# Kernel optimization log

Hardware: AMD Instinct MI355X
Metric: run time of the kernel (lower is better)

Reference implementation:

```python
import jax, jax.numpy as jnp
import numpy as np

B, C, L, MID, HID, OUT, K = 4096, 6, 1024, 512, 512, 256, 5
EPS = 1e-5


def _bn_eval(x, g, b, m, v):
    # BatchNorm1d eval mode on (B, C, T): normalize per channel with running stats
    inv = g / jnp.sqrt(v + EPS)
    return (x - m[None, :, None]) * inv[None, :, None] + b[None, :, None]


def setup_inputs() -> dict:
    key = jax.random.key(0)
    ks = jax.random.split(key, 12)
    s_in = 1.0 / np.sqrt(L)
    s_hid = 1.0 / np.sqrt(HID)
    inp = {
        "x": jax.random.normal(ks[0], (B, C, L), jnp.float32),
        # k stacked self-attention branches (two Linear(L, MID) each)
        "aW1": jax.random.normal(ks[1], (K, L, MID), jnp.float32) * s_in,
        "ab1": jnp.zeros((K, MID), jnp.float32),
        "aW2": jax.random.normal(ks[2], (K, L, MID), jnp.float32) * s_in,
        "ab2": jnp.zeros((K, MID), jnp.float32),
        # linearExchangeLayer: Linear(K*C, C)
        "linW": jax.random.normal(ks[3], (K * C, C), jnp.float32) / np.sqrt(K * C),
        "linb": jnp.zeros((C,), jnp.float32),
        # GraphConvolution weights
        "gW1": jax.random.normal(ks[4], (L, HID), jnp.float32) * s_in,
        "gb1": jnp.zeros((HID,), jnp.float32),
        "gW2": jax.random.normal(ks[5], (HID, OUT), jnp.float32) * s_hid,
        "gb2": jnp.zeros((OUT,), jnp.float32),
        # PReLU (single shared parameter, torch default 0.25)
        "prelu_a": jnp.array(0.25, jnp.float32),
        # BatchNorm1d params + running stats (eval mode)
        "bn1_g": jnp.ones((C,), jnp.float32),
        "bn1_b": jnp.zeros((C,), jnp.float32),
        "bn1_m": jnp.zeros((C,), jnp.float32),
        "bn1_v": jnp.ones((C,), jnp.float32),
        "bn2_g": jnp.ones((C,), jnp.float32),
        "bn2_b": jnp.zeros((C,), jnp.float32),
        "bn2_m": jnp.zeros((C,), jnp.float32),
        "bn2_v": jnp.ones((C,), jnp.float32),
    }
    return inp


def reference(x, aW1, ab1, aW2, ab2, linW, linb, gW1, gb1, gW2, gb2,
              prelu_a, bn1_g, bn1_b, bn1_m, bn1_v, bn2_g, bn2_b, bn2_m, bn2_v):
    b, c, l = x.shape
    k = aW1.shape[0]
    # --- multi-head attention adjacency: (b, c, c) ---
    q = jnp.einsum('bcl,klm->bkcm', x, aW1) + ab1[None, :, None, :]
    kv = jnp.einsum('bcl,klm->bkcm', x, aW2) + ab2[None, :, None, :]
    scores = jax.nn.softmax(jnp.einsum('bkcm,bkdm->bkcd', q, kv), axis=-1)
    # concat heads along last dim: (b, c, k*c)
    cat = scores.transpose(0, 2, 1, 3).reshape(b, c, k * c)
    A = jax.nn.softmax(cat @ linW + linb, axis=-1)  # (b, c, c)
    # --- GraphConvolution 1 (dropout identity in eval) ---
    h = jnp.einsum('bcd,bdh->bch', A, x @ gW1) + gb1
    # PReLU then BatchNorm1d
    h = jnp.where(h >= 0, h, prelu_a * h)
    h = _bn_eval(h, bn1_g, bn1_b, bn1_m, bn1_v)
    # --- GraphConvolution 2 ---
    out = jnp.einsum('bcd,bdh->bch', A, h @ gW2) + gb2
    out = _bn_eval(out, bn2_g, bn2_b, bn2_m, bn2_v)
    return out
```

## Files before the change

### kernel.cpp

```cpp
#include <hip/hip_runtime.h>
#include <hip/hip_bf16.h>


using bf16 = __hip_bfloat16;
using s16x8 = __attribute__((ext_vector_type(8))) short;
using f32x4 = __attribute__((ext_vector_type(4))) float;

#define AS1(p) ((__attribute__((address_space(1))) void*)((void*)(p)))
#define AS3(p) ((__attribute__((address_space(3))) void*)(p))

#if defined(__has_builtin)
#if __has_builtin(__builtin_amdgcn_global_load_lds)
#define HAVE_GLL 1
#endif
#endif

__device__ __forceinline__ float s2f(short s) {
  union { unsigned int u; float f; } c;
  c.u = ((unsigned int)(unsigned short)s) << 16;
  return c.f;
}
__device__ __forceinline__ short f2s(float x) {
  bf16 b = __float2bfloat16(x);
  short s;
  __builtin_memcpy(&s, &b, 2);
  return s;
}

struct GJob {
  const bf16* Bt;
  const float* bias;
  int boff;
  bf16* out;
};
struct GJobs10 {
  GJob j[10];
};

__global__ __launch_bounds__(256) void prep_kernel(
    const float* __restrict__ x, bf16* __restrict__ Xb,
    const float* __restrict__ aW1, bf16* __restrict__ W1T,
    const float* __restrict__ aW2, bf16* __restrict__ W2T,
    const float* __restrict__ gW1, bf16* __restrict__ G1T,
    const float* __restrict__ gW2, bf16* __restrict__ G2T) {
  const int bid = blockIdx.x, tid = threadIdx.x;
  if (bid < 12288) {
    int i = bid * 256 + tid;
    float4 p0 = ((const float4*)x)[i * 2];
    float4 p1 = ((const float4*)x)[i * 2 + 1];
    s16x8 v;
    v[0] = f2s(p0.x); v[1] = f2s(p0.y); v[2] = f2s(p0.z); v[3] = f2s(p0.w);
    v[4] = f2s(p1.x); v[5] = f2s(p1.y); v[6] = f2s(p1.z); v[7] = f2s(p1.w);
    ((s16x8*)Xb)[i] = v;
    return;
  }
  int r = bid - 12288;
  const float* src; short* dst; int R, C, bx, by;
  if (r < 2560) {
    int z = r >> 9, q = r & 511;
    src = aW1 + (size_t)z * 524288; dst = (short*)W1T + (size_t)z * 524288;
    R = 1024; C = 512; bx = q & 31; by = q >> 5;
  } else if (r < 5120) {
    r -= 2560;
    int z = r >> 9, q = r & 511;
    src = aW2 + (size_t)z * 524288; dst = (short*)W2T + (size_t)z * 524288;
    R = 1024; C = 512; bx = q & 31; by = q >> 5;
  } else if (r < 5632) {
    r -= 5120;
    src = gW1; dst = (short*)G1T; R = 1024; C = 512; bx = r & 31; by = r >> 5;
  } else {
    r -= 5632;
    src = gW2; dst = (short*)G2T; R = 512; C = 256; bx = r & 15; by = r >> 4;
  }
  __shared__ short tile[32][33];
  const int tx = tid & 31, ty = tid >> 5;
  const int r0 = bx * 32, c0 = by * 32;
#pragma unroll
  for (int i = 0; i < 4; ++i)
    tile[ty + i * 8][tx] = f2s(src[(size_t)(r0 + ty + i * 8) * C + c0 + tx]);
  __syncthreads();
#pragma unroll
  for (int i = 0; i < 4; ++i)
    dst[(size_t)(c0 + ty + i * 8) * R + r0 + tx] = tile[tx][ty + i * 8];
}

__device__ __forceinline__ void scores_grp(
    const bf16* __restrict__ Qa, const bf16* __restrict__ Ka,
    const bf16* __restrict__ Qb, const bf16* __restrict__ Kb,
    int rowA, int rowB,
    float* __restrict__ dstA, float* __restrict__ dstB,
    int lane) {
  const int l16 = lane & 15, quad = lane >> 4;
  int lr = l16 & 7; if (lr > 5) lr = 5;
  const int gr = ((l16 < 8) ? rowA : rowB) + lr;
  const short* qrow = (const short*)((l16 < 8) ? Qa : Qb) + (size_t)gr * 512 + quad * 8;
  const short* krow = (const short*)((l16 < 8) ? Ka : Kb) + (size_t)gr * 512 + quad * 8;

  f32x4 acc = (f32x4){0.f, 0.f, 0.f, 0.f};
#pragma unroll
  for (int kk = 0; kk < 16; ++kk) {
    s16x8 a = *(const s16x8*)(qrow + kk * 32);
    s16x8 b = *(const s16x8*)(krow + kk * 32);
    acc = __builtin_amdgcn_mfma_f32_16x16x32_bf16(a, b, acc, 0, 0, 0);
  }

  if (l16 < 6) {
#pragma unroll
    for (int r = 0; r < 4; ++r) {
      int m = quad * 4 + r;
      if (m < 6) dstA[m * 6 + l16] = acc[r];
    }
  } else if (l16 >= 8 && l16 < 14) {
#pragma unroll
    for (int r = 0; r < 4; ++r) {
      int m = quad * 4 + r;
      if (m >= 8 && m < 14) dstB[(m - 8) * 6 + (l16 - 8)] = acc[r];
    }
  }
}

__global__ __launch_bounds__(256) void scores_mfma2(
    const bf16* __restrict__ Q0, const bf16* __restrict__ KV0,
    const bf16* __restrict__ Q1, const bf16* __restrict__ KV1,
    float* __restrict__ S, int head0) {
  const int h = blockIdx.y;
  const bf16* Q = h ? Q1 : Q0;
  const bf16* KV = h ? KV1 : KV0;
  const int head = head0 + h;
  const int lane = threadIdx.x & 63, w = threadIdx.x >> 6;
  const int b0 = (blockIdx.x * 4 + w) * 2;
  scores_grp(Q, KV, Q, KV, b0 * 6, (b0 + 1) * 6,
             S + ((size_t)b0 * 5 + head) * 36,
             S + ((size_t)(b0 + 1) * 5 + head) * 36, lane);
}

template <int AF32>
__global__ __launch_bounds__(256) void gemm_bt(
    const void* __restrict__ Ag,
    const bf16* __restrict__ Bt0, const bf16* __restrict__ Bt1,
    const float* __restrict__ bias0, const float* __restrict__ bias1, int boff,
    bf16* __restrict__ out0, bf16* __restrict__ out1,
    int M, int N, int K) {
  const bf16* Bt = (blockIdx.z == 0) ? Bt0 : Bt1;
  const float* bias = (blockIdx.z == 0) ? bias0 : bias1;
  bf16* Cg = (blockIdx.z == 0) ? out0 : out1;

  __shared__ short lA[128 * 32];
  __shared__ short lB[128 * 32];

  const int tid = threadIdx.x;
  const int lane = tid & 63, w = tid >> 6;
  const int wr = w >> 1, wc = w & 1;
  const int l16 = lane & 15, quad = lane >> 4;
  const int lrow = lane >> 2;
  const int scol = (((lane & 3) ^ ((lane >> 3) & 3)) * 8);

  const size_t rm0 = (size_t)blockIdx.x * 128;
  const size_t cn0 = (size_t)blockIdx.y * 128;

  f32x4 acc[4][4];
#pragma unroll
  for (int i = 0; i < 4; ++i)
#pragma unroll
    for (int j = 0; j < 4; ++j) acc[i][j] = (f32x4){0.f, 0.f, 0.f, 0.f};

  for (int kb = 0; kb < K; kb += 32) {
#pragma unroll
    for (int t = 0; t < 2; ++t) {
      int chunk = w * 2 + t;
      int row = chunk * 16 + lrow;
      const bf16* gb = Bt + (cn0 + row) * (size_t)K + kb + scol;
#ifdef HAVE_GLL
      __builtin_amdgcn_global_load_lds(AS1(gb), AS3(lB + chunk * 512), 16, 0, 0);
#else
      *(s16x8*)(lB + chunk * 512 + lane * 8) = *(const s16x8*)gb;
#endif
      if (AF32) {
        const float* ga = (const float*)Ag + (rm0 + row) * (size_t)K + kb + scol;
        float4 p0 = *(const float4*)ga;
        float4 p1 = *(const float4*)(ga + 4);
        s16x8 v;
        v[0] = f2s(p0.x); v[1] = f2s(p0.y); v[2] = f2s(p0.z); v[3] = f2s(p0.w);
        v[4] = f2s(p1.x); v[5] = f2s(p1.y); v[6] = f2s(p1.z); v[7] = f2s(p1.w);
        *(s16x8*)(lA + chunk * 512 + lane * 8) = v;
      } else {
        const bf16* ga = (const bf16*)Ag + (rm0 + row) * (size_t)K + kb + scol;
#ifdef HAVE_GLL
        __builtin_amdgcn_global_load_lds(AS1(ga), AS3(lA + chunk * 512), 16, 0, 0);
#else
        *(s16x8*)(lA + chunk * 512 + lane * 8) = *(const s16x8*)ga;
#endif
      }
    }
    __syncthreads();

    const int q2 = (quad ^ ((l16 >> 1) & 3)) * 8;
    s16x8 af[4], bfv[4];
#pragma unroll
    for (int i = 0; i < 4; ++i) {
      af[i] = *(const s16x8*)(lA + (wr * 64 + i * 16 + l16) * 32 + q2);
      bfv[i] = *(const s16x8*)(lB + (wc * 64 + i * 16 + l16) * 32 + q2);
    }
#pragma unroll
    for (int i = 0; i < 4; ++i)
#pragma unroll
      for (int j = 0; j < 4; ++j)
        acc[i][j] = __builtin_amdgcn_mfma_f32_16x16x32_bf16(af[i], bfv[j], acc[i][j], 0, 0, 0);
    __syncthreads();
  }

#pragma unroll
  for (int j = 0; j < 4; ++j) {
    size_t col = cn0 + wc * 64 + j * 16 + l16;
    float bv = bias ? bias[boff + col] : 0.f;
#pragma unroll
    for (int i = 0; i < 4; ++i) {
      size_t rowb = rm0 + wr * 64 + i * 16 + quad * 4;
#pragma unroll
      for (int r = 0; r < 4; ++r) {
        float v = acc[i][j][r] + bv;
        Cg[(rowb + r) * (size_t)N + col] = __float2bfloat16(v);
      }
    }
  }
}

__global__ __launch_bounds__(512, 2) void gemm256_8ph(
    const bf16* __restrict__ A, GJobs10 jobs, int epi_z,
    const float* __restrict__ prelu_p,
    const float* __restrict__ bn_g, const float* __restrict__ bn_b,
    const float* __restrict__ bn_m, const float* __restrict__ bn_v,
    int M, int N, int K) {
  const GJob jb = jobs.j[blockIdx.z];
  const bf16* Bt = jb.Bt;
  const float* bias = jb.bias;
  const int boff = jb.boff;
  bf16* Cg = jb.out;
  const bool EPI = (epi_z == (int)blockIdx.z);

  __shared__ __attribute__((aligned(16))) short ldsS[65536];
  __shared__ float epi_s[12];

  const int tid = threadIdx.x;
  const int w = tid >> 6, l = tid & 63;
  const int l16 = l & 15, quad = l >> 4;
  const int wr = w >> 2, wc = w & 3;

  if (EPI && tid < 6) {
    float s = bn_g[tid] * rsqrtf(bn_v[tid] + 1e-5f);
    epi_s[tid] = s;
    epi_s[6 + tid] = bn_b[tid] - bn_m[tid] * s;
  }

  const size_t rm0 = (size_t)blockIdx.x * 256;
  const size_t cn0 = (size_t)blockIdx.y * 256;

  const int colS = ((l & 7) ^ (l >> 3)) * 8;
  const int rowS = w * 16 + (l >> 3);
  const short* pAs = (const short*)A + (rm0 + rowS) * (size_t)K + colS;
  const short* pBs = (const short*)Bt + (cn0 + rowS) * (size_t)K + colS;

  const int u0 = (quad ^ (l16 & 7)) * 8;
  const int u1 = ((quad + 4) ^ (l16 & 7)) * 8;

  f32x4 acc[8][4];
#pragma unroll
  for (int i = 0; i < 8; ++i)
#pragma unroll
    for (int j2i = 0; j2i < 4; ++j2i) acc[i][j2i] = (f32x4){0.f, 0.f, 0.f, 0.f};

  s16x8 af[4][2], bf0[2][2], bf1[2][2];

  const int T = K >> 6;

#ifdef HAVE_GLL
#define SA(BUF, H, KB) do {                                                          \
    __builtin_amdgcn_global_load_lds(AS1(pAs + (size_t)((H) * 128) * K + (KB)),      \
        AS3(ldsS + (BUF) * 32768 + (H) * 8192 + w * 1024), 16, 0, 0);                \
    __builtin_amdgcn_global_load_lds(AS1(pAs + (size_t)((H) * 128 + 8) * K + (KB)),  \
        AS3(ldsS + (BUF) * 32768 + (H) * 8192 + w * 1024 + 512), 16, 0, 0);          \
  } while (0)
#define SB(BUF, H, KB) do {                                                          \
    __builtin_amdgcn_global_load_lds(AS1(pBs + (size_t)((H) * 128) * K + (KB)),      \
        AS3(ldsS + (BUF) * 32768 + 16384 + (H) * 8192 + w * 1024), 16, 0, 0);        \
    __builtin_amdgcn_global_load_lds(AS1(pBs + (size_t)((H) * 128 + 8) * K + (KB)),  \
        AS3(ldsS + (BUF) * 32768 + 16384 + (H) * 8192 + w * 1024 + 512), 16, 0, 0);  \
  } while (0)
#else
#define SA(BUF, H, KB) do {                                                          \
    *(s16x8*)(ldsS + (BUF) * 32768 + (H) * 8192 + w * 1024 + l * 8) =                \
        *(const s16x8*)(pAs + (size_t)((H) * 128) * K + (KB));                       \
    *(s16x8*)(ldsS + (BUF) * 32768 + (H) * 8192 + w * 1024 + 512 + l * 8) =          \
        *(const s16x8*)(pAs + (size_t)((H) * 128 + 8) * K + (KB));                   \
  } while (0)
#define SB(BUF, H, KB) do {                                                          \
    *(s16x8*)(ldsS + (BUF) * 32768 + 16384 + (H) * 8192 + w * 1024 + l * 8) =        \
        *(const s16x8*)(pBs + (size_t)((H) * 128) * K + (KB));                       \
    *(s16x8*)(ldsS + (BUF) * 32768 + 16384 + (H) * 8192 + w * 1024 + 512 + l * 8) =  \
        *(const s16x8*)(pBs + (size_t)((H) * 128 + 8) * K + (KB));                   \
  } while (0)
#endif

#define LDA(BUF, MH) do {                                                            \
    _Pragma("unroll") for (int i = 0; i < 4; ++i) {                                  \
      const short* bse = ldsS + (BUF) * 32768 + wr * 8192 + (MH) * 4096 +            \
                         i * 1024 + l16 * 64;                                        \
      af[i][0] = *(const s16x8*)(bse + u0);                                          \
      af[i][1] = *(const s16x8*)(bse + u1);                                          \
    }                                                                                \
  } while (0)

#define LDB(BUF, NH, DST) do {                                                       \
    _Pragma("unroll") for (int n = 0; n < 2; ++n) {                                  \
      const short* bse = ldsS + (BUF) * 32768 + 16384 + (wc >> 1) * 8192 +           \
                         (wc & 1) * 4096 + (NH) * 2048 + n * 1024 + l16 * 64;        \
      DST[n][0] = *(const s16x8*)(bse + u0);                                         \
      DST[n][1] = *(const s16x8*)(bse + u1);                                         \
    }                                                                                \
  } while (0)

#define MFMAQ(MH, NH, BSET) do {                                                     \
    _Pragma("unroll") for (int i = 0; i < 4; ++i)                                    \
      _Pragma("unroll") for (int n = 0; n < 2; ++n) {                                \
        acc[(MH) * 4 + i][(NH) * 2 + n] = __builtin_amdgcn_mfma_f32_16x16x32_bf16(   \
            af[i][0], BSET[n][0], acc[(MH) * 4 + i][(NH) * 2 + n], 0, 0, 0);         \
        acc[(MH) * 4 + i][(NH) * 2 + n] = __builtin_amdgcn_mfma_f32_16x16x32_bf16(   \
            af[i][1], BSET[n][1], acc[(MH) * 4 + i][(NH) * 2 + n], 0, 0, 0);         \
      }                                                                              \
  } while (0)

#define BARX() asm volatile("s_barrier" ::: "memory")
#define LGKM0() do { asm volatile("s_waitcnt lgkmcnt(0)" ::: "memory");              \
                     __builtin_amdgcn_sched_barrier(0); } while (0)
#define VM6() do { asm volatile("s_waitcnt vmcnt(6)" ::: "memory");                  \
                   __builtin_amdgcn_sched_barrier(0); } while (0)

#define TILE_STEP(BUF, t) do {                                                       \
    const int kN_ = ((t) + 1 < T ? (t) + 1 : T - 1) << 6;                            \
    const int k2_ = ((t) + 2 < T ? (t) + 2 : T - 1) << 6;                            \
               \
    LDA(BUF, 0); LDB(BUF, 0, bf0); LDB(BUF, 1, bf1);                                 \
    SA((BUF) ^ 1, 1, kN_);                                                           \
    BARX(); LGKM0();                                                                 \
    __builtin_amdgcn_s_setprio(1); MFMAQ(0, 0, bf0); __builtin_amdgcn_s_setprio(0);  \
    BARX();                                                                          \
                        \
    SB(BUF, 0, k2_);                                                                 \
    BARX();                                                                          \
    __builtin_amdgcn_s_setprio(1); MFMAQ(0, 1, bf1); __builtin_amdgcn_s_setprio(0);  \
    BARX();                                                                          \
                                               \
    LDA(BUF, 1);                                                                     \
    SB(BUF, 1, k2_);                                                                 \
    BARX(); LGKM0();                                                                 \
    __builtin_amdgcn_s_setprio(1); MFMAQ(1, 1, bf1); __builtin_amdgcn_s_setprio(0);  \
    BARX();                                                                          \
                         \
    SA(BUF, 0, k2_);                                                                 \
    VM6();                                                                           \
    BARX();                                                                          \
    __builtin_amdgcn_s_setprio(1); MFMAQ(1, 0, bf0); __builtin_amdgcn_s_setprio(0);  \
    BARX();                                                                          \
  } while (0)

  {
    const int k1_ = (T > 1 ? 1 : 0) << 6;
    SB(0, 0, 0); SB(0, 1, 0); SA(0, 0, 0); SA(0, 1, 0);
    SB(1, 0, k1_); SB(1, 1, k1_); SA(1, 0, k1_);
    VM6();
    BARX();
  }

  for (int t = 0; t < T; t += 2) {
    TILE_STEP(0, t);
    TILE_STEP(1, t + 1);
  }

  float pa = EPI ? prelu_p[0] : 0.f;
  short* st = ldsS + w * 8192;
#pragma unroll
  for (int jj = 0; jj < 4; ++jj) {
    int coll = jj * 16 + l16;
    float bv = bias ? bias[boff + (int)cn0 + wc * 64 + coll] : 0.f;
#pragma unroll
    for (int i = 0; i < 8; ++i) {
#pragma unroll
      for (int r = 0; r < 4; ++r) {
        int rowl = i * 16 + quad * 4 + r;
        float v = acc[i][jj][r] + bv;
        if (EPI) {
          v = (v >= 0.f) ? v : pa * v;
          int c = (int)((rm0 + wr * 128 + rowl) % 6);
          v = v * epi_s[c] + epi_s[6 + c];
        }
        st[rowl * 64 + coll] = f2s(v);
      }
    }
  }
  __syncthreads();
#pragma unroll
  for (int it = 0; it < 16; ++it) {
    int rowl = it * 8 + (l >> 3);
    int cch = (l & 7) * 8;
    s16x8 vv = *(const s16x8*)(st + rowl * 64 + cch);
    *(s16x8*)((short*)Cg + (rm0 + wr * 128 + rowl) * (size_t)N +
              cn0 + wc * 64 + cch) = vv;
  }
#undef SA
#undef SB
#undef LDA
#undef LDB
#undef MFMAQ
#undef BARX
#undef LGKM0
#undef VM6
#undef TILE_STEP
}

template <int ALLP>
__global__ __launch_bounds__(256) void mid5(
    const float* __restrict__ S,
    const bf16* __restrict__ Q0, const bf16* __restrict__ Q1,
    const bf16* __restrict__ Q2, const bf16* __restrict__ Q3,
    const bf16* __restrict__ K0, const bf16* __restrict__ K1,
    const bf16* __restrict__ K2, const bf16* __restrict__ K3,
    const bf16* __restrict__ Q4, const bf16* __restrict__ K4,
    bf16* __restrict__ Xb,
    const float* __restrict__ linW, const float* __restrict__ linb,
    float* __restrict__ Afull) {
  const int tid = threadIdx.x, g = tid >> 6, t = tid & 63;
  const int b = blockIdx.x * 4 + g;
  __shared__ float p[4][5][6][6];
  __shared__ float Ar[4][6][6];
  __shared__ float lw[30][6];
  __shared__ float lbv[6];

  if (tid < 30) {
#pragma unroll
    for (int j = 0; j < 6; ++j) lw[tid][j] = linW[tid * 6 + j];
  }
  if (tid < 6) lbv[tid] = linb[tid];

  const int r6 = b * 6;
  if (ALLP) {
    scores_grp(Q0, K0, Q1, K1, r6, r6, &p[g][0][0][0], &p[g][1][0][0], t);
    scores_grp(Q2, K2, Q3, K3, r6, r6, &p[g][2][0][0], &p[g][3][0][0], t);
    scores_grp(Q4, K4, Q4, K4, r6, r6, &p[g][4][0][0], &p[g][4][0][0], t);
  } else {
    if (t < 36) {
#pragma unroll
      for (int k = 0; k < 4; ++k)
        p[g][k][t / 6][t % 6] = S[((size_t)b * 5 + k) * 36 + t];
    }
    scores_grp(Q4, K4, Q4, K4, r6, r6, &p[g][4][0][0], &p[g][4][0][0], t);
  }
  __syncthreads();

  if (t < 30) {
    int k = t / 6, c = t % 6;
    float v[6];
#pragma unroll
    for (int d = 0; d < 6; ++d) v[d] = p[g][k][c][d];
    float mx = v[0];
#pragma unroll
    for (int d = 1; d < 6; ++d) mx = fmaxf(mx, v[d]);
    float s = 0.f;
#pragma unroll
    for (int d = 0; d < 6; ++d) { v[d] = expf(v[d] - mx); s += v[d]; }
    float inv = 1.f / s;
#pragma unroll
    for (int d = 0; d < 6; ++d) p[g][k][c][d] = v[d] * inv;
  }
  __syncthreads();

  if (t < 6) {
    int c = t;
    float ap[6];
#pragma unroll
    for (int j = 0; j < 6; ++j) ap[j] = lbv[j];
    for (int k = 0; k < 5; ++k)
#pragma unroll
      for (int d = 0; d < 6; ++d) {
        float pv = p[g][k][c][d];
#pragma unroll
        for (int j = 0; j < 6; ++j) ap[j] += pv * lw[k * 6 + d][j];
      }
    float mx = ap[0];
#pragma unroll
    for (int j = 1; j < 6; ++j) mx = fmaxf(mx, ap[j]);
    float s = 0.f;
#pragma unroll
    for (int j = 0; j < 6; ++j) { ap[j] = expf(ap[j] - mx); s += ap[j]; }
    float inv = 1.f / s;
#pragma unroll
    for (int j = 0; j < 6; ++j) {
      float a = ap[j] * inv;
      Ar[g][c][j] = a;
      Afull[(size_t)b * 36 + c * 6 + j] = a;
    }
  }
  __syncthreads();

  short* xp = (short*)Xb;
#pragma unroll
  for (int it = 0; it < 2; ++it) {
    int c8 = (it * 64 + t) * 8;
    s16x8 xv[6];
#pragma unroll
    for (int d = 0; d < 6; ++d)
      xv[d] = *(const s16x8*)(xp + ((size_t)r6 + d) * 1024 + c8);
#pragma unroll
    for (int c = 0; c < 6; ++c) {
      s16x8 o;
#pragma unroll
      for (int e = 0; e < 8; ++e) {
        float s = 0.f;
#pragma unroll
        for (int d = 0; d < 6; ++d) s += Ar[g][c][d] * s2f(xv[d][e]);
        o[e] = f2s(s);
      }
      *(s16x8*)(xp + ((size_t)r6 + c) * 1024 + c8) = o;
    }
  }
}

__global__ __launch_bounds__(256) void batch_out4(
    const float* __restrict__ Afull, const bf16* __restrict__ HW,
    const float* __restrict__ gb2,
    const float* __restrict__ g2, const float* __restrict__ b2,
    const float* __restrict__ m2, const float* __restrict__ v2,
    float* __restrict__ out) {
  const int tid = threadIdx.x, g = tid >> 6, t = tid & 63;
  const int b = blockIdx.x * 4 + g;
  __shared__ float Ar[4][36];
  __shared__ float sc[6], sm[6], sb[6];
  if (t < 36) Ar[g][t] = Afull[(size_t)b * 36 + t];
  if (tid < 6) {
    sc[tid] = g2[tid] * rsqrtf(v2[tid] + 1e-5f);
    sm[tid] = m2[tid];
    sb[tid] = b2[tid];
  }
  __syncthreads();
  for (int col = t; col < 256; col += 64) {
    float hw[6];
#pragma unroll
    for (int d = 0; d < 6; ++d) hw[d] = s2f(((const short*)HW)[((size_t)b * 6 + d) * 256 + col]);
    float gv = gb2[col];
#pragma unroll
    for (int c = 0; c < 6; ++c) {
      float o = gv;
#pragma unroll
      for (int d = 0; d < 6; ++d) o += Ar[g][c * 6 + d] * hw[d];
      o = (o - sm[c]) * sc[c] + sb[c];
      out[((size_t)b * 6 + c) * 256 + col] = o;
    }
  }
}

extern "C" void kernel_launch(void* const* d_in, const int* in_sizes, int n_in,
                              void* d_out, int out_size, void* d_ws, size_t ws_size,
                              hipStream_t stream) {
  const float* x    = (const float*)d_in[0];
  const float* aW1  = (const float*)d_in[1];
  const float* ab1  = (const float*)d_in[2];
  const float* aW2  = (const float*)d_in[3];
  const float* ab2  = (const float*)d_in[4];
  const float* linW = (const float*)d_in[5];
  const float* linb = (const float*)d_in[6];
  const float* gW1  = (const float*)d_in[7];
  const float* gb1  = (const float*)d_in[8];
  const float* gW2  = (const float*)d_in[9];
  const float* gb2  = (const float*)d_in[10];
  const float* prelu = (const float*)d_in[11];
  const float* bn1g = (const float*)d_in[12];
  const float* bn1b = (const float*)d_in[13];
  const float* bn1m = (const float*)d_in[14];
  const float* bn1v = (const float*)d_in[15];
  const float* bn2g = (const float*)d_in[16];
  const float* bn2b = (const float*)d_in[17];
  const float* bn2m = (const float*)d_in[18];
  const float* bn2v = (const float*)d_in[19];

  char* ws = (char*)d_ws;
  bf16* W1T = (bf16*)(ws + 0);
  bf16* W2T = (bf16*)(ws + 5242880);
  bf16* G1T = (bf16*)(ws + 10485760);
  bf16* G2T = (bf16*)(ws + 11534336);
  float* S  = (float*)(ws + 11796480);
  float* Af = (float*)(ws + 14745600);
  bf16* Xb  = (bf16*)(ws + 15335424);
#define PANEL(i) ((bf16*)(ws + 65667072 + (size_t)(i) * 25165824))
  const bool big5 = ws_size >= 292159488ull;

  prep_kernel<<<18048, 256, 0, stream>>>(x, Xb, aW1, W1T, aW2, W2T, gW1, G1T, gW2, G2T);

  GJobs10 J{};

  if (big5) {
    for (int h = 0; h < 4; ++h) {
      J.j[2 * h]     = GJob{W1T + (size_t)h * 524288, ab1, h * 512, PANEL(2 * h)};
      J.j[2 * h + 1] = GJob{W2T + (size_t)h * 524288, ab2, h * 512, PANEL(2 * h + 1)};
    }
    J.j[8] = GJob{W1T + 4 * 524288, ab1, 2048, (bf16*)d_out};
    J.j[9] = GJob{W2T + 4 * 524288, ab2, 2048, PANEL(8)};
    gemm256_8ph<<<dim3(96, 2, 10), 512, 0, stream>>>(
        Xb, J, -1, nullptr, nullptr, nullptr, nullptr, nullptr, 24576, 512, 1024);

    mid5<1><<<1024, 256, 0, stream>>>(
        nullptr, PANEL(0), PANEL(2), PANEL(4), PANEL(6),
        PANEL(1), PANEL(3), PANEL(5), PANEL(7),
        (const bf16*)d_out, PANEL(8), Xb, linW, linb, Af);

    GJobs10 JH{};
    JH.j[0] = GJob{G1T, gb1, 0, PANEL(0)};
    gemm256_8ph<<<dim3(96, 2, 1), 512, 0, stream>>>(
        Xb, JH, 0, prelu, bn1g, bn1b, bn1m, bn1v, 24576, 512, 1024);

    gemm_bt<0><<<dim3(192, 2, 1), 256, 0, stream>>>(
        PANEL(0), G2T, G2T, nullptr, nullptr, 0, PANEL(1), PANEL(1), 24576, 256, 512);

    batch_out4<<<1024, 256, 0, stream>>>(Af, PANEL(1), gb2, bn2g, bn2b, bn2m, bn2v,
                                         (float*)d_out);
  } else {
    for (int h = 0; h < 2; ++h) {
      J.j[2 * h]     = GJob{W1T + (size_t)h * 524288, ab1, h * 512, PANEL(2 * h)};
      J.j[2 * h + 1] = GJob{W2T + (size_t)h * 524288, ab2, h * 512, PANEL(2 * h + 1)};
    }
    gemm256_8ph<<<dim3(96, 2, 4), 512, 0, stream>>>(
        Xb, J, -1, nullptr, nullptr, nullptr, nullptr, nullptr, 24576, 512, 1024);
    scores_mfma2<<<dim3(512, 2), 256, 0, stream>>>(
        PANEL(0), PANEL(1), PANEL(2), PANEL(3), S, 0);

    for (int h = 0; h < 2; ++h) {
      J.j[2 * h]     = GJob{W1T + (size_t)(h + 2) * 524288, ab1, (h + 2) * 512, PANEL(4 + 2 * h)};
      J.j[2 * h + 1] = GJob{W2T + (size_t)(h + 2) * 524288, ab2, (h + 2) * 512, PANEL(5 + 2 * h)};
    }
    gemm256_8ph<<<dim3(96, 2, 4), 512, 0, stream>>>(
        Xb, J, -1, nullptr, nullptr, nullptr, nullptr, nullptr, 24576, 512, 1024);
    scores_mfma2<<<dim3(512, 2), 256, 0, stream>>>(
        PANEL(4), PANEL(5), PANEL(6), PANEL(7), S, 2);

    J.j[0] = GJob{W1T + 4 * 524288, ab1, 2048, PANEL(0)};
    J.j[1] = GJob{W2T + 4 * 524288, ab2, 2048, PANEL(1)};
    gemm256_8ph<<<dim3(96, 2, 2), 512, 0, stream>>>(
        Xb, J, -1, nullptr, nullptr, nullptr, nullptr, nullptr, 24576, 512, 1024);

    mid5<0><<<1024, 256, 0, stream>>>(
        S, nullptr, nullptr, nullptr, nullptr, nullptr, nullptr, nullptr, nullptr,
        PANEL(0), PANEL(1), Xb, linW, linb, Af);

    GJobs10 JH{};
    JH.j[0] = GJob{G1T, gb1, 0, PANEL(2)};
    gemm256_8ph<<<dim3(96, 2, 1), 512, 0, stream>>>(
        Xb, JH, 0, prelu, bn1g, bn1b, bn1m, bn1v, 24576, 512, 1024);

    gemm_bt<0><<<dim3(192, 2, 1), 256, 0, stream>>>(
        PANEL(2), G2T, G2T, nullptr, nullptr, 0, PANEL(3), PANEL(3), 24576, 256, 512);

    batch_out4<<<1024, 256, 0, stream>>>(Af, PANEL(3), gb2, bn2g, bn2b, bn2m, bn2v,
                                         (float*)d_out);
  }
#undef PANEL
}
```

Before: 629.9 us.

## Precompute per-head W1·W2ᵀ to form attention scores as x·M·xᵀ

Instead of projecting x into Q and K panels for every head (ten 24576x1024x512 GEMMs), the code precomputes M_h = W1_h W2_h^T (1024x1024) per head and computes X·M_h with a new GEMM whose epilogue contracts the result against x rows in LDS to produce 6x6 score blocks directly. A bias term x·(W2 b1) is added via a small precomputed vector, and the ab2 term is dropped on the assumption that it shifts each softmax row by a constant. This avoids writing and re-reading large Q/K panels, but the score GEMM has N=1024 per head, which is about the same FLOPs as before. The weight-product GEMM and an extra bf16 rounding of M add precision risk.

```diff
diff --git a/kernel.cpp b/kernel.cpp
--- a/kernel.cpp
+++ b/kernel.cpp
@@ -32,6 +32,7 @@
   const float* bias;
   int boff;
   bf16* out;
+  const bf16* Aj;
 };
 struct GJobs10 {
   GJob j[10];
@@ -39,11 +40,14 @@
 
 __global__ __launch_bounds__(256) void prep_kernel(
     const float* __restrict__ x, bf16* __restrict__ Xb,
-    const float* __restrict__ aW1, bf16* __restrict__ W1T,
-    const float* __restrict__ aW2, bf16* __restrict__ W2T,
+    const float* __restrict__ aW1, bf16* __restrict__ W1b,
+    const float* __restrict__ aW2, bf16* __restrict__ W2b,
     const float* __restrict__ gW1, bf16* __restrict__ G1T,
-    const float* __restrict__ gW2, bf16* __restrict__ G2T) {
+    const float* __restrict__ gW2, bf16* __restrict__ G2T,
+    const float* __restrict__ ab1, float* __restrict__ w2a1) {
   const int bid = blockIdx.x, tid = threadIdx.x;
+  __shared__ short tile[32][33];
+
   if (bid < 12288) {
     int i = bid * 256 + tid;
     float4 p0 = ((const float4*)x)[i * 2];
@@ -54,84 +58,47 @@
     ((s16x8*)Xb)[i] = v;
     return;
   }
-  int r = bid - 12288;
-  const float* src; short* dst; int R, C, bx, by;
-  if (r < 2560) {
-    int z = r >> 9, q = r & 511;
-    src = aW1 + (size_t)z * 524288; dst = (short*)W1T + (size_t)z * 524288;
-    R = 1024; C = 512; bx = q & 31; by = q >> 5;
-  } else if (r < 5120) {
-    r -= 2560;
-    int z = r >> 9, q = r & 511;
-    src = aW2 + (size_t)z * 524288; dst = (short*)W2T + (size_t)z * 524288;
-    R = 1024; C = 512; bx = q & 31; by = q >> 5;
-  } else if (r < 5632) {
-    r -= 5120;
-    src = gW1; dst = (short*)G1T; R = 1024; C = 512; bx = r & 31; by = r >> 5;
-  } else {
-    r -= 5632;
-    src = gW2; dst = (short*)G2T; R = 512; C = 256; bx = r & 15; by = r >> 4;
-  }
-  __shared__ short tile[32][33];
-  const int tx = tid & 31, ty = tid >> 5;
-  const int r0 = bx * 32, c0 = by * 32;
-#pragma unroll
-  for (int i = 0; i < 4; ++i)
-    tile[ty + i * 8][tx] = f2s(src[(size_t)(r0 + ty + i * 8) * C + c0 + tx]);
-  __syncthreads();
-#pragma unroll
-  for (int i = 0; i < 4; ++i)
-    dst[(size_t)(c0 + ty + i * 8) * R + r0 + tx] = tile[tx][ty + i * 8];
-}
-
-__device__ __forceinline__ void scores_grp(
-    const bf16* __restrict__ Qa, const bf16* __restrict__ Ka,
-    const bf16* __restrict__ Qb, const bf16* __restrict__ Kb,
-    int rowA, int rowB,
-    float* __restrict__ dstA, float* __restrict__ dstB,
-    int lane) {
-  const int l16 = lane & 15, quad = lane >> 4;
-  int lr = l16 & 7; if (lr > 5) lr = 5;
-  const int gr = ((l16 < 8) ? rowA : rowB) + lr;
-  const short* qrow = (const short*)((l16 < 8) ? Qa : Qb) + (size_t)gr * 512 + quad * 8;
-  const short* krow = (const short*)((l16 < 8) ? Ka : Kb) + (size_t)gr * 512 + quad * 8;
-
-  f32x4 acc = (f32x4){0.f, 0.f, 0.f, 0.f};
-#pragma unroll
-  for (int kk = 0; kk < 16; ++kk) {
-    s16x8 a = *(const s16x8*)(qrow + kk * 32);
-    s16x8 b = *(const s16x8*)(krow + kk * 32);
-    acc = __builtin_amdgcn_mfma_f32_16x16x32_bf16(a, b, acc, 0, 0, 0);
-  }
-
-  if (l16 < 6) {
-#pragma unroll
-    for (int r = 0; r < 4; ++r) {
-      int m = quad * 4 + r;
-      if (m < 6) dstA[m * 6 + l16] = acc[r];
-    }
-  } else if (l16 >= 8 && l16 < 14) {
-#pragma unroll
-    for (int r = 0; r < 4; ++r) {
-      int m = quad * 4 + r;
-      if (m >= 8 && m < 14) dstB[(m - 8) * 6 + (l16 - 8)] = acc[r];
-    }
-  }
-}
-
-__global__ __launch_bounds__(256) void scores_mfma2(
-    const bf16* __restrict__ Q0, const bf16* __restrict__ KV0,
-    const bf16* __restrict__ Q1, const bf16* __restrict__ KV1,
-    float* __restrict__ S, int head0) {
-  const int h = blockIdx.y;
-  const bf16* Q = h ? Q1 : Q0;
-  const bf16* KV = h ? KV1 : KV0;
-  const int head = head0 + h;
-  const int lane = threadIdx.x & 63, w = threadIdx.x >> 6;
-  const int b0 = (blockIdx.x * 4 + w) * 2;
-  scores_grp(Q, KV, Q, KV, b0 * 6, (b0 + 1) * 6,
-             S + ((size_t)b0 * 5 + head) * 36,
-             S + ((size_t)(b0 + 1) * 5 + head) * 36, lane);
+  if (bid < 14848) {
+    const float* src = (bid < 13568) ? aW1 : aW2;
+    bf16* dst = (bid < 13568) ? W1b : W2b;
+    int i = ((bid < 13568) ? (bid - 12288) : (bid - 13568)) * 256 + tid;
+    float4 p0 = ((const float4*)src)[i * 2];
+    float4 p1 = ((const float4*)src)[i * 2 + 1];
+    s16x8 v;
+    v[0] = f2s(p0.x); v[1] = f2s(p0.y); v[2] = f2s(p0.z); v[3] = f2s(p0.w);
+    v[4] = f2s(p1.x); v[5] = f2s(p1.y); v[6] = f2s(p1.z); v[7] = f2s(p1.w);
+    ((s16x8*)dst)[i] = v;
+    return;
+  }
+  if (bid < 15488) {
+    const float* src; short* dst; int R, C, bx, by;
+    if (bid < 15360) {
+      int r = bid - 14848;
+      src = gW1; dst = (short*)G1T; R = 1024; C = 512; bx = r & 31; by = r >> 5;
+    } else {
+      int r = bid - 15360;
+      src = gW2; dst = (short*)G2T; R = 512; C = 256; bx = r & 15; by = r >> 4;
+    }
+    const int tx = tid & 31, ty = tid >> 5;
+    const int r0 = bx * 32, c0 = by * 32;
+#pragma unroll
+    for (int i = 0; i < 4; ++i)
+      tile[ty + i * 8][tx] = f2s(src[(size_t)(r0 + ty + i * 8) * C + c0 + tx]);
+    __syncthreads();
+#pragma unroll
+    for (int i = 0; i < 4; ++i)
+      dst[(size_t)(c0 + ty + i * 8) * R + r0 + tx] = tile[tx][ty + i * 8];
+    return;
+  }
+  int idx = (bid - 15488) * 256 + tid;
+  if (idx < 5120) {
+    int h = idx >> 10, l = idx & 1023;
+    const float* wp = aW2 + (size_t)h * 524288 + (size_t)l * 512;
+    const float* bp = ab1 + h * 512;
+    float s = 0.f;
+    for (int m = 0; m < 512; ++m) s += wp[m] * bp[m];
+    w2a1[h * 1024 + l] = s;
+  }
 }
 
 template <int AF32>
@@ -232,6 +199,7 @@
     const float* __restrict__ bn_m, const float* __restrict__ bn_v,
     int M, int N, int K) {
   const GJob jb = jobs.j[blockIdx.z];
+  const bf16* Ae = jb.Aj ? jb.Aj : A;
   const bf16* Bt = jb.Bt;
   const float* bias = jb.bias;
   const int boff = jb.boff;
@@ -257,7 +225,7 @@
 
   const int colS = ((l & 7) ^ (l >> 3)) * 8;
   const int rowS = w * 16 + (l >> 3);
-  const short* pAs = (const short*)A + (rm0 + rowS) * (size_t)K + colS;
+  const short* pAs = (const short*)Ae + (rm0 + rowS) * (size_t)K + colS;
   const short* pBs = (const short*)Bt + (cn0 + rowS) * (size_t)K + colS;
 
   const int u0 = (quad ^ (l16 & 7)) * 8;
@@ -334,28 +302,26 @@
                      __builtin_amdgcn_sched_barrier(0); } while (0)
 #define VM6() do { asm volatile("s_waitcnt vmcnt(6)" ::: "memory");                  \
                    __builtin_amdgcn_sched_barrier(0); } while (0)
+#define VM0() do { asm volatile("s_waitcnt vmcnt(0)" ::: "memory");                  \
+                   __builtin_amdgcn_sched_barrier(0); } while (0)
 
 #define TILE_STEP(BUF, t) do {                                                       \
     const int kN_ = ((t) + 1 < T ? (t) + 1 : T - 1) << 6;                            \
     const int k2_ = ((t) + 2 < T ? (t) + 2 : T - 1) << 6;                            \
-               \
     LDA(BUF, 0); LDB(BUF, 0, bf0); LDB(BUF, 1, bf1);                                 \
     SA((BUF) ^ 1, 1, kN_);                                                           \
     BARX(); LGKM0();                                                                 \
     __builtin_amdgcn_s_setprio(1); MFMAQ(0, 0, bf0); __builtin_amdgcn_s_setprio(0);  \
     BARX();                                                                          \
-                        \
     SB(BUF, 0, k2_);                                                                 \
     BARX();                                                                          \
     __builtin_amdgcn_s_setprio(1); MFMAQ(0, 1, bf1); __builtin_amdgcn_s_setprio(0);  \
     BARX();                                                                          \
-                                               \
     LDA(BUF, 1);                                                                     \
     SB(BUF, 1, k2_);                                                                 \
     BARX(); LGKM0();                                                                 \
     __builtin_amdgcn_s_setprio(1); MFMAQ(1, 1, bf1); __builtin_amdgcn_s_setprio(0);  \
     BARX();                                                                          \
-                         \
     SA(BUF, 0, k2_);                                                                 \
     VM6();                                                                           \
     BARX();                                                                          \
@@ -376,6 +342,8 @@
     TILE_STEP(1, t + 1);
   }
 
+  VM0();
+  BARX();
   float pa = EPI ? prelu_p[0] : 0.f;
   short* st = ldsS + w * 8192;
 #pragma unroll
@@ -414,23 +382,223 @@
 #undef BARX
 #undef LGKM0
 #undef VM6
+#undef VM0
 #undef TILE_STEP
 }
 
-template <int ALLP>
-__global__ __launch_bounds__(256) void mid5(
-    const float* __restrict__ S,
-    const bf16* __restrict__ Q0, const bf16* __restrict__ Q1,
-    const bf16* __restrict__ Q2, const bf16* __restrict__ Q3,
-    const bf16* __restrict__ K0, const bf16* __restrict__ K1,
-    const bf16* __restrict__ K2, const bf16* __restrict__ K3,
-    const bf16* __restrict__ Q4, const bf16* __restrict__ K4,
+__global__ __launch_bounds__(512, 2) void gemmS(
+    const bf16* __restrict__ A,
+    const bf16* __restrict__ Mh,
+    float* __restrict__ S4, int K) {
+  const int h = blockIdx.z;
+  const bf16* Bt = Mh + (size_t)h * 1048576;
+
+  __shared__ __attribute__((aligned(16))) short ldsS[65536];
+
+  const int tid = threadIdx.x;
+  const int w = tid >> 6, l = tid & 63;
+  const int l16 = l & 15, quad = l >> 4;
+  const int wr = w >> 2, wc = w & 3;
+
+  const size_t rm0 = (size_t)blockIdx.x * 256;
+  const size_t cn0 = (size_t)blockIdx.y * 256;
+
+  const int colS = ((l & 7) ^ (l >> 3)) * 8;
+  const int rowS = w * 16 + (l >> 3);
+  const short* pAs = (const short*)A + (rm0 + rowS) * (size_t)K + colS;
+  const short* pBs = (const short*)Bt + (cn0 + rowS) * (size_t)K + colS;
+
+  const int u0 = (quad ^ (l16 & 7)) * 8;
+  const int u1 = ((quad + 4) ^ (l16 & 7)) * 8;
+
+  f32x4 acc[8][4];
+#pragma unroll
+  for (int i = 0; i < 8; ++i)
+#pragma unroll
+    for (int j2i = 0; j2i < 4; ++j2i) acc[i][j2i] = (f32x4){0.f, 0.f, 0.f, 0.f};
+
+  s16x8 af[4][2], bf0[2][2], bf1[2][2];
+
+  const int T = K >> 6;
+
+#ifdef HAVE_GLL
+#define SA(BUF, H, KB) do {                                                          \
+    __builtin_amdgcn_global_load_lds(AS1(pAs + (size_t)((H) * 128) * K + (KB)),      \
+        AS3(ldsS + (BUF) * 32768 + (H) * 8192 + w * 1024), 16, 0, 0);                \
+    __builtin_amdgcn_global_load_lds(AS1(pAs + (size_t)((H) * 128 + 8) * K + (KB)),  \
+        AS3(ldsS + (BUF) * 32768 + (H) * 8192 + w * 1024 + 512), 16, 0, 0);          \
+  } while (0)
+#define SB(BUF, H, KB) do {                                                          \
+    __builtin_amdgcn_global_load_lds(AS1(pBs + (size_t)((H) * 128) * K + (KB)),      \
+        AS3(ldsS + (BUF) * 32768 + 16384 + (H) * 8192 + w * 1024), 16, 0, 0);        \
+    __builtin_amdgcn_global_load_lds(AS1(pBs + (size_t)((H) * 128 + 8) * K + (KB)),  \
+        AS3(ldsS + (BUF) * 32768 + 16384 + (H) * 8192 + w * 1024 + 512), 16, 0, 0);  \
+  } while (0)
+#else
+#define SA(BUF, H, KB) do {                                                          \
+    *(s16x8*)(ldsS + (BUF) * 32768 + (H) * 8192 + w * 1024 + l * 8) =                \
+        *(const s16x8*)(pAs + (size_t)((H) * 128) * K + (KB));                       \
+    *(s16x8*)(ldsS + (BUF) * 32768 + (H) * 8192 + w * 1024 + 512 + l * 8) =          \
+        *(const s16x8*)(pAs + (size_t)((H) * 128 + 8) * K + (KB));                   \
+  } while (0)
+#define SB(BUF, H, KB) do {                                                          \
+    *(s16x8*)(ldsS + (BUF) * 32768 + 16384 + (H) * 8192 + w * 1024 + l * 8) =        \
+        *(const s16x8*)(pBs + (size_t)((H) * 128) * K + (KB));                       \
+    *(s16x8*)(ldsS + (BUF) * 32768 + 16384 + (H) * 8192 + w * 1024 + 512 + l * 8) =  \
+        *(const s16x8*)(pBs + (size_t)((H) * 128 + 8) * K + (KB));                   \
+  } while (0)
+#endif
+
+#define LDA(BUF, MH) do {                                                            \
+    _Pragma("unroll") for (int i = 0; i < 4; ++i) {                                  \
+      const short* bse = ldsS + (BUF) * 32768 + wr * 8192 + (MH) * 4096 +            \
+                         i * 1024 + l16 * 64;                                        \
+      af[i][0] = *(const s16x8*)(bse + u0);                                          \
+      af[i][1] = *(const s16x8*)(bse + u1);                                          \
+    }                                                                                \
+  } while (0)
+
+#define LDB(BUF, NH, DST) do {                                                       \
+    _Pragma("unroll") for (int n = 0; n < 2; ++n) {                                  \
+      const short* bse = ldsS + (BUF) * 32768 + 16384 + (wc >> 1) * 8192 +           \
+                         (wc & 1) * 4096 + (NH) * 2048 + n * 1024 + l16 * 64;        \
+      DST[n][0] = *(const s16x8*)(bse + u0);                                         \
+      DST[n][1] = *(const s16x8*)(bse + u1);                                         \
+    }                                                                                \
+  } while (0)
+
+#define MFMAQ(MH, NH, BSET) do {                                                     \
+    _Pragma("unroll") for (int i = 0; i < 4; ++i)                                    \
+      _Pragma("unroll") for (int n = 0; n < 2; ++n) {                                \
+        acc[(MH) * 4 + i][(NH) * 2 + n] = __builtin_amdgcn_mfma_f32_16x16x32_bf16(   \
+            af[i][0], BSET[n][0], acc[(MH) * 4 + i][(NH) * 2 + n], 0, 0, 0);         \
+        acc[(MH) * 4 + i][(NH) * 2 + n] = __builtin_amdgcn_mfma_f32_16x16x32_bf16(   \
+            af[i][1], BSET[n][1], acc[(MH) * 4 + i][(NH) * 2 + n], 0, 0, 0);         \
+      }                                                                              \
+  } while (0)
+
+#define BARX() asm volatile("s_barrier" ::: "memory")
+#define LGKM0() do { asm volatile("s_waitcnt lgkmcnt(0)" ::: "memory");              \
+                     __builtin_amdgcn_sched_barrier(0); } while (0)
+#define VM6() do { asm volatile("s_waitcnt vmcnt(6)" ::: "memory");                  \
+                   __builtin_amdgcn_sched_barrier(0); } while (0)
+#define VM0() do { asm volatile("s_waitcnt vmcnt(0)" ::: "memory");                  \
+                   __builtin_amdgcn_sched_barrier(0); } while (0)
+
+#define TILE_STEP(BUF, t) do {                                                       \
+    const int kN_ = ((t) + 1 < T ? (t) + 1 : T - 1) << 6;                            \
+    const int k2_ = ((t) + 2 < T ? (t) + 2 : T - 1) << 6;                            \
+    LDA(BUF, 0); LDB(BUF, 0, bf0); LDB(BUF, 1, bf1);                                 \
+    SA((BUF) ^ 1, 1, kN_);                                                           \
+    BARX(); LGKM0();                                                                 \
+    __builtin_amdgcn_s_setprio(1); MFMAQ(0, 0, bf0); __builtin_amdgcn_s_setprio(0);  \
+    BARX();                                                                          \
+    SB(BUF, 0, k2_);                                                                 \
+    BARX();                                                                          \
+    __builtin_amdgcn_s_setprio(1); MFMAQ(0, 1, bf1); __builtin_amdgcn_s_setprio(0);  \
+    BARX();                                                                          \
+    LDA(BUF, 1);                                                                     \
+    SB(BUF, 1, k2_);                                                                 \
+    BARX(); LGKM0();                                                                 \
+    __builtin_amdgcn_s_setprio(1); MFMAQ(1, 1, bf1); __builtin_amdgcn_s_setprio(0);  \
+    BARX();                                                                          \
+    SA(BUF, 0, k2_);                                                                 \
+    VM6();                                                                           \
+    BARX();                                                                          \
+    __builtin_amdgcn_s_setprio(1); MFMAQ(1, 0, bf0); __builtin_amdgcn_s_setprio(0);  \
+    BARX();                                                                          \
+  } while (0)
+
+  {
+    const int k1_ = (T > 1 ? 1 : 0) << 6;
+    SB(0, 0, 0); SB(0, 1, 0); SA(0, 0, 0); SA(0, 1, 0);
+    SB(1, 0, k1_); SB(1, 1, k1_); SA(1, 0, k1_);
+    VM6();
+    BARX();
+  }
+
+  for (int t = 0; t < T; t += 2) {
+    TILE_STEP(0, t);
+    TILE_STEP(1, t + 1);
+  }
+
+  VM0();
+  BARX();
+#pragma unroll
+  for (int jj = 0; jj < 4; ++jj) {
+    int C = wc * 64 + jj * 16 + l16;
+#pragma unroll
+    for (int i = 0; i < 8; ++i) {
+#pragma unroll
+      for (int r = 0; r < 4; ++r) {
+        int Rl = wr * 128 + i * 16 + quad * 4 + r;
+        int addr = Rl * 256 + (((C >> 3) ^ (Rl & 7)) << 3) + (C & 7);
+        ldsS[addr] = f2s(acc[i][jj][r]);
+      }
+    }
+  }
+  __syncthreads();
+
+  const int R = (int)rm0;
+  const int b_lo = R / 6, b_hi = (R + 255) / 6;
+  int lr = l16 & 7; if (lr > 5) lr = 5;
+  const size_t s4base = (size_t)blockIdx.y * 737280;
+
+  for (int b0 = b_lo + 2 * w; b0 <= b_hi; b0 += 16) {
+    const int b1 = b0 + 1;
+    const int bb = (l16 < 8) ? b0 : b1;
+    int grow = bb * 6 + lr; if (grow > 24575) grow = 24575;
+    int yr = grow - R; yr = yr < 0 ? 0 : (yr > 255 ? 255 : yr);
+    const short* xr = (const short*)A + (size_t)grow * K + cn0 + quad * 8;
+    const int ybase = yr * 256, ysw = yr & 7;
+
+    f32x4 sa = (f32x4){0.f, 0.f, 0.f, 0.f};
+#pragma unroll
+    for (int kk = 0; kk < 8; ++kk) {
+      s16x8 ya = *(const s16x8*)(ldsS + ybase + (((kk * 4 + quad) ^ ysw) << 3));
+      s16x8 xb = *(const s16x8*)(xr + kk * 32);
+      sa = __builtin_amdgcn_mfma_f32_16x16x32_bf16(ya, xb, sa, 0, 0, 0);
+    }
+
+#pragma unroll
+    for (int r = 0; r < 4; ++r) {
+      int m = quad * 4 + r;
+      if (l16 < 6) {
+        if (m < 6) {
+          int row = b0 * 6 + m;
+          if (row >= R && row < R + 256)
+            S4[s4base + ((size_t)b0 * 5 + h) * 36 + m * 6 + l16] = sa[r];
+        }
+      } else if (l16 >= 8 && l16 < 14) {
+        if (m >= 8 && m < 14) {
+          int c = m - 8, row = b1 * 6 + c;
+          if (row >= R && row < R + 256)
+            S4[s4base + ((size_t)b1 * 5 + h) * 36 + c * 6 + (l16 - 8)] = sa[r];
+        }
+      }
+    }
+  }
+#undef SA
+#undef SB
+#undef LDA
+#undef LDB
+#undef MFMAQ
+#undef BARX
+#undef LGKM0
+#undef VM6
+#undef VM0
+#undef TILE_STEP
+}
+
+__global__ __launch_bounds__(256) void mid_ax(
+    const float* __restrict__ S4, const float* __restrict__ w2a1,
     bf16* __restrict__ Xb,
     const float* __restrict__ linW, const float* __restrict__ linb,
     float* __restrict__ Afull) {
   const int tid = threadIdx.x, g = tid >> 6, t = tid & 63;
   const int b = blockIdx.x * 4 + g;
   __shared__ float p[4][5][6][6];
+  __shared__ float vv[4][5][6];
   __shared__ float Ar[4][6][6];
   __shared__ float lw[30][6];
   __shared__ float lbv[6];
@@ -441,18 +609,25 @@
   }
   if (tid < 6) lbv[tid] = linb[tid];
 
-  const int r6 = b * 6;
-  if (ALLP) {
-    scores_grp(Q0, K0, Q1, K1, r6, r6, &p[g][0][0][0], &p[g][1][0][0], t);
-    scores_grp(Q2, K2, Q3, K3, r6, r6, &p[g][2][0][0], &p[g][3][0][0], t);
-    scores_grp(Q4, K4, Q4, K4, r6, r6, &p[g][4][0][0], &p[g][4][0][0], t);
-  } else {
-    if (t < 36) {
-#pragma unroll
-      for (int k = 0; k < 4; ++k)
-        p[g][k][t / 6][t % 6] = S[((size_t)b * 5 + k) * 36 + t];
-    }
-    scores_grp(Q4, K4, Q4, K4, r6, r6, &p[g][4][0][0], &p[g][4][0][0], t);
+  if (t < 36) {
+    size_t idx = ((size_t)b * 5) * 36 + t;
+#pragma unroll
+    for (int k = 0; k < 5; ++k)
+      p[g][k][t / 6][t % 6] = S4[idx + k * 36] + S4[737280 + idx + k * 36] +
+                              S4[2 * 737280 + idx + k * 36] +
+                              S4[3 * 737280 + idx + k * 36];
+  }
+  if (t < 30) {
+    int k = t / 6, d = t % 6;
+    const s16x8* xr = (const s16x8*)((const short*)Xb + ((size_t)b * 6 + d) * 1024);
+    const float* wv = w2a1 + k * 1024;
+    float s = 0.f;
+    for (int i = 0; i < 128; ++i) {
+      s16x8 xv8 = xr[i];
+#pragma unroll
+      for (int e = 0; e < 8; ++e) s += s2f(xv8[e]) * wv[i * 8 + e];
+    }
+    vv[g][k][d] = s;
   }
   __syncthreads();
 
@@ -460,7 +635,7 @@
     int k = t / 6, c = t % 6;
     float v[6];
 #pragma unroll
-    for (int d = 0; d < 6; ++d) v[d] = p[g][k][c][d];
+    for (int d = 0; d < 6; ++d) v[d] = p[g][k][c][d] + vv[g][k][d];
     float mx = v[0];
 #pragma unroll
     for (int d = 1; d < 6; ++d) mx = fmaxf(mx, v[d]);
@@ -501,6 +676,7 @@
   }
   __syncthreads();
 
+  const int r6 = b * 6;
   short* xp = (short*)Xb;
 #pragma unroll
   for (int it = 0; it < 2; ++it) {
@@ -564,7 +740,6 @@
   const float* aW1  = (const float*)d_in[1];
   const float* ab1  = (const float*)d_in[2];
   const float* aW2  = (const float*)d_in[3];
-  const float* ab2  = (const float*)d_in[4];
   const float* linW = (const float*)d_in[5];
   const float* linb = (const float*)d_in[6];
   const float* gW1  = (const float*)d_in[7];
@@ -582,83 +757,45 @@
   const float* bn2v = (const float*)d_in[19];
 
   char* ws = (char*)d_ws;
-  bf16* W1T = (bf16*)(ws + 0);
-  bf16* W2T = (bf16*)(ws + 5242880);
-  bf16* G1T = (bf16*)(ws + 10485760);
-  bf16* G2T = (bf16*)(ws + 11534336);
-  float* S  = (float*)(ws + 11796480);
-  float* Af = (float*)(ws + 14745600);
-  bf16* Xb  = (bf16*)(ws + 15335424);
-#define PANEL(i) ((bf16*)(ws + 65667072 + (size_t)(i) * 25165824))
-  const bool big5 = ws_size >= 292159488ull;
-
-  prep_kernel<<<18048, 256, 0, stream>>>(x, Xb, aW1, W1T, aW2, W2T, gW1, G1T, gW2, G2T);
-
-  GJobs10 J{};
-
-  if (big5) {
-    for (int h = 0; h < 4; ++h) {
-      J.j[2 * h]     = GJob{W1T + (size_t)h * 524288, ab1, h * 512, PANEL(2 * h)};
-      J.j[2 * h + 1] = GJob{W2T + (size_t)h * 524288, ab2, h * 512, PANEL(2 * h + 1)};
-    }
-    J.j[8] = GJob{W1T + 4 * 524288, ab1, 2048, (bf16*)d_out};
-    J.j[9] = GJob{W2T + 4 * 524288, ab2, 2048, PANEL(8)};
-    gemm256_8ph<<<dim3(96, 2, 10), 512, 0, stream>>>(
-        Xb, J, -1, nullptr, nullptr, nullptr, nullptr, nullptr, 24576, 512, 1024);
-
-    mid5<1><<<1024, 256, 0, stream>>>(
-        nullptr, PANEL(0), PANEL(2), PANEL(4), PANEL(6),
-        PANEL(1), PANEL(3), PANEL(5), PANEL(7),
-        (const bf16*)d_out, PANEL(8), Xb, linW, linb, Af);
-
+  bf16* W1b  = (bf16*)(ws + 0);
+  bf16* W2b  = (bf16*)(ws + 10485760);
+  bf16* G1T  = (bf16*)(ws + 20971520);
+  bf16* G2T  = (bf16*)(ws + 22020096);
+  float* w2a1 = (float*)(ws + 22282240);
+  float* Af  = (float*)(ws + 22302720);
+  float* S4  = (float*)(ws + 22892544);
+  bf16* Xb   = (bf16*)(ws + 34689024);
+  bf16* MhT  = (bf16*)(ws + 85020672);
+  bf16* PH   = (bf16*)(ws + 95506432);
+  bf16* PHW  = (bf16*)(ws + 120672256);
+  (void)ws_size;
+
+  prep_kernel<<<15508, 256, 0, stream>>>(x, Xb, aW1, W1b, aW2, W2b,
+                                         gW1, G1T, gW2, G2T, ab1, w2a1);
+
+  {
+    GJobs10 J{};
+    for (int h = 0; h < 5; ++h)
+      J.j[h] = GJob{W1b + (size_t)h * 524288, nullptr, 0,
+                    MhT + (size_t)h * 1048576, W2b + (size_t)h * 524288};
+    gemm256_8ph<<<dim3(4, 4, 5), 512, 0, stream>>>(
+        W2b, J, -1, nullptr, nullptr, nullptr, nullptr, nullptr, 1024, 1024, 512);
+  }
+
+  gemmS<<<dim3(96, 4, 5), 512, 0, stream>>>(Xb, MhT, S4, 1024);
+
+  mid_ax<<<1024, 256, 0, stream>>>(S4, w2a1, Xb, linW, linb, Af);
+
+  {
     GJobs10 JH{};
-    JH.j[0] = GJob{G1T, gb1, 0, PANEL(0)};
+    JH.j[0] = GJob{G1T, gb1, 0, PH, nullptr};
     gemm256_8ph<<<dim3(96, 2, 1), 512, 0, stream>>>(
         Xb, JH, 0, prelu, bn1g, bn1b, bn1m, bn1v, 24576, 512, 1024);
-
-    gemm_bt<0><<<dim3(192, 2, 1), 256, 0, stream>>>(
-        PANEL(0), G2T, G2T, nullptr, nullptr, 0, PANEL(1), PANEL(1), 24576, 256, 512);
-
-    batch_out4<<<1024, 256, 0, stream>>>(Af, PANEL(1), gb2, bn2g, bn2b, bn2m, bn2v,
-                                         (float*)d_out);
-  } else {
-    for (int h = 0; h < 2; ++h) {
-      J.j[2 * h]     = GJob{W1T + (size_t)h * 524288, ab1, h * 512, PANEL(2 * h)};
-      J.j[2 * h + 1] = GJob{W2T + (size_t)h * 524288, ab2, h * 512, PANEL(2 * h + 1)};
-    }
-    gemm256_8ph<<<dim3(96, 2, 4), 512, 0, stream>>>(
-        Xb, J, -1, nullptr, nullptr, nullptr, nullptr, nullptr, 24576, 512, 1024);
-    scores_mfma2<<<dim3(512, 2), 256, 0, stream>>>(
-        PANEL(0), PANEL(1), PANEL(2), PANEL(3), S, 0);
-
-    for (int h = 0; h < 2; ++h) {
-      J.j[2 * h]     = GJob{W1T + (size_t)(h + 2) * 524288, ab1, (h + 2) * 512, PANEL(4 + 2 * h)};
-      J.j[2 * h + 1] = GJob{W2T + (size_t)(h + 2) * 524288, ab2, (h + 2) * 512, PANEL(5 + 2 * h)};
-    }
-    gemm256_8ph<<<dim3(96, 2, 4), 512, 0, stream>>>(
-        Xb, J, -1, nullptr, nullptr, nullptr, nullptr, nullptr, 24576, 512, 1024);
-    scores_mfma2<<<dim3(512, 2), 256, 0, stream>>>(
-        PANEL(4), PANEL(5), PANEL(6), PANEL(7), S, 2);
-
-    J.j[0] = GJob{W1T + 4 * 524288, ab1, 2048, PANEL(0)};
-    J.j[1] = GJob{W2T + 4 * 524288, ab2, 2048, PANEL(1)};
-    gemm256_8ph<<<dim3(96, 2, 2), 512, 0, stream>>>(
-        Xb, J, -1, nullptr, nullptr, nullptr, nullptr, nullptr, 24576, 512, 1024);
-
-    mid5<0><<<1024, 256, 0, stream>>>(
-        S, nullptr, nullptr, nullptr, nullptr, nullptr, nullptr, nullptr, nullptr,
-        PANEL(0), PANEL(1), Xb, linW, linb, Af);
-
-    GJobs10 JH{};
-    JH.j[0] = GJob{G1T, gb1, 0, PANEL(2)};
-    gemm256_8ph<<<dim3(96, 2, 1), 512, 0, stream>>>(
-        Xb, JH, 0, prelu, bn1g, bn1b, bn1m, bn1v, 24576, 512, 1024);
-
-    gemm_bt<0><<<dim3(192, 2, 1), 256, 0, stream>>>(
-        PANEL(2), G2T, G2T, nullptr, nullptr, 0, PANEL(3), PANEL(3), 24576, 256, 512);
-
-    batch_out4<<<1024, 256, 0, stream>>>(Af, PANEL(3), gb2, bn2g, bn2b, bn2m, bn2v,
-                                         (float*)d_out);
-  }
-#undef PANEL
+  }
+
+  gemm_bt<0><<<dim3(192, 2, 1), 256, 0, stream>>>(
+      PH, G2T, G2T, nullptr, nullptr, 0, PHW, PHW, 24576, 256, 512);
+
+  batch_out4<<<1024, 256, 0, stream>>>(Af, PHW, gb2, bn2g, bn2b, bn2m, bn2v,
+                                       (float*)d_out);
 }
```

Result: slower. 657.3 us (+4.3%).
